# Performance work log

Hardware: AMD Instinct MI355X
Metric: run time of the kernel (lower is better)

Reference implementation:

```python
import jax, jax.numpy as jnp
import numpy as np

N = 200000      # total nodes
E = 800000      # directed edges
G = 4096        # graphs in batch
D_DRUG = 128
D_CELL = 954
HID = 128
OUT = 128
EPS = 1e-5      # BatchNorm eps


def _bn(x, gamma, beta):
    # training-mode BatchNorm1d (batch statistics, biased var), dropout is eval/identity
    m = jnp.mean(x, axis=0)
    v = jnp.mean((x - m) ** 2, axis=0)
    return gamma * (x - m) * jax.lax.rsqrt(v + EPS) + beta


def _gcn_conv(x, edge_index, W, b):
    # PyG GCNConv: add self-loops, symmetric normalization, aggregate, then bias
    src = jnp.concatenate([edge_index[0], jnp.arange(N)])
    dst = jnp.concatenate([edge_index[1], jnp.arange(N)])
    ones = jnp.ones(src.shape[0], dtype=x.dtype)
    deg = jax.ops.segment_sum(ones, dst, num_segments=N)
    dinv = jnp.where(deg > 0, jax.lax.rsqrt(jnp.maximum(deg, 1.0)), 0.0)
    norm = dinv[src] * dinv[dst]                      # [E+N]
    h = x @ W                                         # [N, out]
    msg = h[src] * norm[:, None]                      # gather + scale
    out = jax.ops.segment_sum(msg, dst, num_segments=N)  # scatter-add
    return out + b


def setup_inputs() -> dict:
    key = jax.random.key(0)
    ks = jax.random.split(key, 12)
    x = jax.random.normal(ks[0], (N, D_DRUG), jnp.float32)
    edge_index = jax.random.randint(ks[1], (2, E), 0, N)
    ibatch = (jnp.arange(N) * G) // N  # sorted, every graph non-empty
    gexpr = jax.random.normal(ks[2], (G, D_CELL), jnp.float32)

    def w(k, shape):
        return jax.random.normal(k, shape, jnp.float32) / np.float32(np.sqrt(shape[0]))

    return {
        "x": x, "edge_index": edge_index, "ibatch": ibatch, "gexpr": gexpr,
        "W1": w(ks[3], (D_DRUG, HID)), "b1": jnp.zeros((HID,), jnp.float32),
        "g1": jnp.ones((HID,), jnp.float32), "be1": jnp.zeros((HID,), jnp.float32),
        "W2": w(ks[4], (HID, OUT)), "b2": jnp.zeros((OUT,), jnp.float32),
        "g2": jnp.ones((OUT,), jnp.float32), "be2": jnp.zeros((OUT,), jnp.float32),
        "Wc1": w(ks[5], (D_CELL, HID)), "bc1": jnp.zeros((HID,), jnp.float32),
        "gc": jnp.ones((HID,), jnp.float32), "bec": jnp.zeros((HID,), jnp.float32),
        "Wc2": w(ks[6], (HID, OUT)), "bc2": jnp.zeros((OUT,), jnp.float32),
    }


def reference(x, edge_index, ibatch, gexpr,
              W1, b1, g1, be1, W2, b2, g2, be2,
              Wc1, bc1, gc, bec, Wc2, bc2):
    # drug branch
    h = _gcn_conv(x, edge_index, W1, b1)
    h = _bn(jax.nn.relu(h), g1, be1)
    h = _gcn_conv(h, edge_index, W2, b2)
    h = _bn(jax.nn.relu(h), g2, be2)
    x_drug = jax.ops.segment_max(h, ibatch, num_segments=G)  # global_max_pool
    # cellline branch
    c = jnp.tanh(gexpr @ Wc1 + bc1)
    c = _bn(c, gc, bec)
    x_cell = jax.nn.relu(c @ Wc2 + bc2)
    return x_drug, x_cell
```

## Files before the change

kernel.cpp:

```cpp
#include <hip/hip_runtime.h>

#define NFEAT 128

typedef __attribute__((ext_vector_type(4))) float f32x4;
typedef __attribute__((ext_vector_type(8))) short bf16x8;

__device__ __forceinline__ unsigned short f2bf(float f) {
    unsigned u = __builtin_bit_cast(unsigned, f);
    u += 0x7fffu + ((u >> 16) & 1u);
    return (unsigned short)(u >> 16);
}
__device__ __forceinline__ float bf2f(unsigned short s) {
    unsigned u = ((unsigned)s) << 16;
    return __builtin_bit_cast(float, u);
}

__device__ __forceinline__ void dma16(const void* g, void* l) {
    __builtin_amdgcn_global_load_lds(
        (const __attribute__((address_space(1))) unsigned int*)g,
        (__attribute__((address_space(3))) unsigned int*)l, 16, 0, 0);
}

template <int ACT, typename OutT, typename AT>
__device__ __forceinline__ void gemm_body(
    int bx, int by, const AT* __restrict__ A, const unsigned short* __restrict__ Bt,
    OutT* __restrict__ C, int M, int ldA, int ldB,
    const float* __restrict__ bias, const float* __restrict__ dscale, char* smem)
{
    constexpr bool AF32 = (sizeof(AT) == 4);
    AT* ash = (AT*)smem;
    const int tid = threadIdx.x;
    const int wv = tid >> 6, lane = tid & 63;
    const int l16 = lane & 15, quad = lane >> 4;
    const int kbase = by * 128;
    const long tile0 = (long)bx * 64;

    const int nc0 = (wv & 1) * 64;
    bf16x8 bfr[4][4];
#pragma unroll
    for (int nt = 0; nt < 4; ++nt) {
        const unsigned short* bp =
            Bt + (size_t)(nc0 + nt * 16 + l16) * ldB + kbase + quad * 8;
#pragma unroll
        for (int ks = 0; ks < 4; ++ks)
            bfr[nt][ks] = *(const bf16x8*)(bp + ks * 32);
    }

    {
        const int r0 = wv * 16;
        if constexpr (AF32) {
#pragma unroll
            for (int j = 0; j < 8; ++j) {
                const float* gp = (const float*)A +
                    (size_t)(tile0 + r0 + j * 2 + (lane >> 5)) * ldA + kbase +
                    (lane & 31) * 4;
                dma16(gp, (void*)&ash[(r0 + j * 2) * 128]);
            }
        } else {
#pragma unroll
            for (int j = 0; j < 4; ++j) {
                const unsigned short* gp = (const unsigned short*)A +
                    (size_t)(tile0 + r0 + j * 4 + (lane >> 4)) * ldA + kbase +
                    l16 * 8;
                dma16(gp, (void*)&ash[(r0 + j * 4) * 128]);
            }
        }
    }
    __syncthreads();

    const int rh = wv >> 1;
    bf16x8 af[2][4];
#pragma unroll
    for (int mt = 0; mt < 2; ++mt) {
        const int row = rh * 32 + mt * 16 + l16;
#pragma unroll
        for (int ks = 0; ks < 4; ++ks) {
            if constexpr (AF32) {
                const float* lp = (const float*)&ash[0] + row * 128 + ks * 32 + quad * 8;
                f32x4 v0 = *(const f32x4*)lp;
                f32x4 v1 = *(const f32x4*)(lp + 4);
                bf16x8 t;
                t[0] = (short)f2bf(v0[0]); t[1] = (short)f2bf(v0[1]);
                t[2] = (short)f2bf(v0[2]); t[3] = (short)f2bf(v0[3]);
                t[4] = (short)f2bf(v1[0]); t[5] = (short)f2bf(v1[1]);
                t[6] = (short)f2bf(v1[2]); t[7] = (short)f2bf(v1[3]);
                af[mt][ks] = t;
            } else {
                af[mt][ks] = *(const bf16x8*)((const unsigned short*)&ash[0] +
                                              row * 128 + ks * 32 + quad * 8);
            }
        }
    }

    f32x4 acc[2][4];
#pragma unroll
    for (int a = 0; a < 2; ++a)
#pragma unroll
        for (int b = 0; b < 4; ++b) acc[a][b] = (f32x4){0.f, 0.f, 0.f, 0.f};
#pragma unroll
    for (int ks = 0; ks < 4; ++ks)
#pragma unroll
        for (int nt = 0; nt < 4; ++nt)
#pragma unroll
            for (int mt = 0; mt < 2; ++mt)
                acc[mt][nt] = __builtin_amdgcn_mfma_f32_16x16x32_bf16(
                    af[mt][ks], bfr[nt][ks], acc[mt][nt], 0, 0, 0);

    C += (size_t)by * M * NFEAT;
    float ds[2][4];
#pragma unroll
    for (int mt = 0; mt < 2; ++mt)
#pragma unroll
        for (int r = 0; r < 4; ++r) {
            long row = tile0 + rh * 32 + mt * 16 + quad * 4 + r;
            ds[mt][r] = dscale ? dscale[row] : 1.f;
        }
#pragma unroll
    for (int nt = 0; nt < 4; ++nt) {
        int col = nc0 + nt * 16 + l16;
        float bv = bias ? bias[col] : 0.f;
#pragma unroll
        for (int mt = 0; mt < 2; ++mt) {
            long rbase = tile0 + rh * 32 + mt * 16 + quad * 4;
#pragma unroll
            for (int r = 0; r < 4; ++r) {
                float v = acc[mt][nt][r] + bv;
                if (ACT == 1) v = tanhf(v);
                if (ACT == 2) v = fmaxf(v, 0.f);
                v *= ds[mt][r];
                if constexpr (sizeof(OutT) == 2)
                    C[(size_t)(rbase + r) * NFEAT + col] = (OutT)f2bf(v);
                else
                    C[(size_t)(rbase + r) * NFEAT + col] = (OutT)v;
            }
        }
    }
}

__global__ void k_prep(const float* __restrict__ W1, unsigned short* __restrict__ W1t,
                       const float* __restrict__ Wc1, unsigned short* __restrict__ Wc1t,
                       const float* __restrict__ gexpr, float* __restrict__ Apad,
                       const int* __restrict__ dst, int* __restrict__ deg,
                       int G, int DC, int DCP, int E, int r1, int r2, int r3)
{
    int b = blockIdx.x, t = threadIdx.x;
    if (b < r1) {
        int idx = b * 256 + t;
        int n = idx >> 7, k = idx & 127;
        W1t[idx] = f2bf(W1[(size_t)k * NFEAT + n]);
    } else if (b < r2) {
        int idx = (b - r1) * 256 + t;
        int n = idx >> 10, k = idx & 1023;
        Wc1t[idx] = (k < DC) ? f2bf(Wc1[(size_t)k * NFEAT + n]) : (unsigned short)0;
    } else if (b < r3) {
        long idx = (long)(b - r2) * 256 + t;
        if (idx < (long)G * DCP) {
            long i = idx / DCP; int k = (int)(idx - i * DCP);
            Apad[idx] = (k < DC) ? gexpr[i * DC + k] : 0.f;
        }
    } else {
        int e = (b - r3) * 256 + t;
        if (e < E) atomicAdd(&deg[dst[e]], 1);
    }
}

__device__ __forceinline__ void bnfold_body(
    int bb, const float* __restrict__ sums8, const float* __restrict__ gamma,
    const float* __restrict__ beta, float invN,
    const float* __restrict__ W, const float* __restrict__ extra,
    unsigned short* __restrict__ Wt, float* __restrict__ brow)
{
    __shared__ float ssc[128], ssh[128];
    int t = threadIdx.x;
    if (t < 128) {
        float s = 0.f, s2 = 0.f;
#pragma unroll
        for (int c = 0; c < 8; ++c) { s += sums8[c * 256 + t]; s2 += sums8[c * 256 + 128 + t]; }
        float mean = s * invN;
        float var = s2 * invN - mean * mean;
        float rstd = rsqrtf(fmaxf(var, 0.f) + 1e-5f);
        float sc = gamma[t] * rstd;
        ssc[t] = sc;
        ssh[t] = beta[t] - mean * sc;
    }
    __syncthreads();
    if (bb < 64) {
        int idx = bb * 256 + t;
        int n = idx >> 7, k = idx & 127;
        Wt[idx] = f2bf(W[(size_t)k * NFEAT + n] * ssc[k]);
    } else if (t < 128) {
        float s = extra ? extra[t] : 0.f;
        for (int k = 0; k < 128; ++k) s += ssh[k] * W[(size_t)k * NFEAT + t];
        brow[t] = s;
    }
}

__global__ void k_bnfold2(
    const float* sA, const float* gA, const float* bA, float invA,
    const float* WA, const float* eA, unsigned short* WtA, float* browA,
    const float* sB, const float* gB, const float* bB, float invB,
    const float* WB, const float* eB, unsigned short* WtB, float* browB)
{
    int b = blockIdx.x;
    if (b < 65) bnfold_body(b, sA, gA, bA, invA, WA, eA, WtA, browA);
    else        bnfold_body(b - 65, sB, gB, bB, invB, WB, eB, WtB, browB);
}

__global__ __launch_bounds__(256) void k_scan1(const int* __restrict__ deg,
        int* __restrict__ rowptr, int* __restrict__ bsum, float* __restrict__ dinv, int N)
{
    __shared__ int sh[256];
    int t = threadIdx.x;
    int base = blockIdx.x * 1024 + t * 4;
    int v[4];
#pragma unroll
    for (int j = 0; j < 4; ++j) {
        v[j] = (base + j < N) ? deg[base + j] : 0;
        if (base + j < N) dinv[base + j] = rsqrtf((float)(v[j] + 1));
    }
    int s = v[0] + v[1] + v[2] + v[3];
    sh[t] = s;
    __syncthreads();
    int incl = s;
    for (int off = 1; off < 256; off <<= 1) {
        int x = (t >= off) ? sh[t - off] : 0;
        __syncthreads();
        incl += x;
        sh[t] = incl;
        __syncthreads();
    }
    int run = incl - s;
#pragma unroll
    for (int j = 0; j < 4; ++j) {
        if (base + j < N) rowptr[base + j] = run;
        run += v[j];
    }
    if (t == 255) bsum[blockIdx.x] = incl;
}

__global__ void k_scan2(int* __restrict__ bsum, int nb)
{
    __shared__ int sh[256];
    int t = threadIdx.x;
    int s = (t < nb) ? bsum[t] : 0;
    sh[t] = s;
    __syncthreads();
    int incl = s;
    for (int off = 1; off < 256; off <<= 1) {
        int x = (t >= off) ? sh[t - off] : 0;
        __syncthreads();
        incl += x;
        sh[t] = incl;
        __syncthreads();
    }
    if (t < nb) bsum[t] = incl - s;
}

__global__ void k_scan3(int* __restrict__ rowptr, int* __restrict__ cursor,
                        const int* __restrict__ bsum, int N, int E)
{
    int i = blockIdx.x * 256 + threadIdx.x;
    if (i < N) {
        int v = rowptr[i] + bsum[i >> 10];
        rowptr[i] = v;
        cursor[i] = v;
    } else if (i == N) {
        rowptr[N] = E;
    }
}

__global__ __launch_bounds__(256) void k_pair1(
    const int* __restrict__ src, const int* __restrict__ dst,
    int* __restrict__ cursor, int* __restrict__ csr, int E,
    const float* __restrict__ x, const unsigned short* __restrict__ W1t,
    unsigned short* __restrict__ h, int N, const float* __restrict__ dinv,
    const float* __restrict__ Apad, const unsigned short* __restrict__ Wc1t,
    float* __restrict__ pbuf, int G, int nf, int nd)
{
    extern __shared__ char smem[];
    int b = blockIdx.x;
    if (b < nf) {
        int e = b * 256 + threadIdx.x;
        if (e < E) {
            int pos = atomicAdd(&cursor[dst[e]], 1);
            csr[pos] = src[e];
        }
    } else if (b < nf + nd) {
        gemm_body<0, unsigned short, float>(b - nf, 0, x, W1t, h, N, 128, 128,
                                            nullptr, dinv, smem);
    } else {
        int idx = b - nf - nd;
        gemm_body<0, float, float>(idx & 63, idx >> 6, Apad, Wc1t, pbuf, G,
                                   1024, 1024, nullptr, nullptr, smem);
    }
}

__device__ __forceinline__ void unpack_add(float* acc, uint4 a)
{
    acc[0] += bf2f((unsigned short)(a.x & 0xffff));
    acc[1] += bf2f((unsigned short)(a.x >> 16));
    acc[2] += bf2f((unsigned short)(a.y & 0xffff));
    acc[3] += bf2f((unsigned short)(a.y >> 16));
    acc[4] += bf2f((unsigned short)(a.z & 0xffff));
    acc[5] += bf2f((unsigned short)(a.z >> 16));
    acc[6] += bf2f((unsigned short)(a.w & 0xffff));
    acc[7] += bf2f((unsigned short)(a.w >> 16));
}

__device__ __forceinline__ void row_gather(const unsigned short* __restrict__ h,
    const int* __restrict__ rowptr, const int* __restrict__ csr,
    long i, int f, float* acc)
{
    int lo = rowptr[i], hi = rowptr[i + 1];
    int e = lo;
    for (; e + 3 < hi; e += 4) {
        int s0 = csr[e], s1 = csr[e + 1], s2 = csr[e + 2], s3 = csr[e + 3];
        uint4 a = *(const uint4*)(h + ((size_t)s0 << 7) + f);
        uint4 b = *(const uint4*)(h + ((size_t)s1 << 7) + f);
        uint4 c = *(const uint4*)(h + ((size_t)s2 << 7) + f);
        uint4 d = *(const uint4*)(h + ((size_t)s3 << 7) + f);
        unpack_add(acc, a); unpack_add(acc, b);
        unpack_add(acc, c); unpack_add(acc, d);
    }
    for (; e < hi; ++e) {
        int s0 = csr[e];
        uint4 a = *(const uint4*)(h + ((size_t)s0 << 7) + f);
        unpack_add(acc, a);
    }
    uint4 hs = *(const uint4*)(h + ((size_t)i << 7) + f);
    unpack_add(acc, hs);
}

__global__ __launch_bounds__(256) void k_pair2(
    const unsigned short* __restrict__ h, const int* __restrict__ rowptr,
    const int* __restrict__ csr, const float* __restrict__ dinv,
    const float* __restrict__ bias, unsigned short* __restrict__ out,
    float* __restrict__ sums8, int N, int na,
    const float* __restrict__ p, const float* __restrict__ biasC,
    unsigned short* __restrict__ cbuf, float* __restrict__ sumsC, int G)
{
    __shared__ float red[4][256];
    const int tid = threadIdx.x;
    if (blockIdx.x >= na) {
        int bb = blockIdx.x - na;
        int j = tid & 127;
        int slot = bb * 2 + (tid >> 7);
        const int nslots = 64;
        const size_t st = (size_t)G * NFEAT;
        float b = biasC[j], s = 0.f, s2 = 0.f;
        for (int i = slot; i < G; i += nslots) {
            size_t o = (size_t)i * NFEAT + j;
            float v = b;
#pragma unroll
            for (int c = 0; c < 8; ++c) v += p[o + c * st];
            v = tanhf(v);
            cbuf[o] = f2bf(v);
            s += v; s2 += v * v;
        }
        atomicAdd(&sumsC[(bb & 7) * 256 + j], s);
        atomicAdd(&sumsC[(bb & 7) * 256 + 128 + j], s2);
        return;
    }
    const int wv = tid >> 6, lane = tid & 63;
    const int f = (tid & 15) << 3;
    const long g0 = (long)blockIdx.x * 16 + (tid >> 4);
    const long gstride = (long)na * 16;

    f32x4 b0 = *(const f32x4*)&bias[f];
    f32x4 b1 = *(const f32x4*)&bias[f + 4];

    float s8[8], q8[8];
#pragma unroll
    for (int j = 0; j < 8; ++j) { s8[j] = 0.f; q8[j] = 0.f; }

    for (long i = g0; i < N; i += gstride) {
        float acc[8];
#pragma unroll
        for (int j = 0; j < 8; ++j) acc[j] = 0.f;
        row_gather(h, rowptr, csr, i, f, acc);

        float di = dinv[i];
        unsigned short o[8];
#pragma unroll
        for (int j = 0; j < 8; ++j) {
            float bj = (j < 4) ? b0[j] : b1[j - 4];
            float v = fmaxf(di * acc[j] + bj, 0.f);
            o[j] = f2bf(v);
            s8[j] += v; q8[j] += v * v;
        }
        *(uint4*)(out + (i << 7) + f) = *(const uint4*)o;
    }

#pragma unroll
    for (int j = 0; j < 8; ++j) {
        s8[j] += __shfl_xor(s8[j], 16);
        s8[j] += __shfl_xor(s8[j], 32);
        q8[j] += __shfl_xor(q8[j], 16);
        q8[j] += __shfl_xor(q8[j], 32);
    }
    if (lane < 16) {
#pragma unroll
        for (int j = 0; j < 8; ++j) {
            red[wv][f + j] = s8[j];
            red[wv][128 + f + j] = q8[j];
        }
    }
    __syncthreads();
    float tot = red[0][tid] + red[1][tid] + red[2][tid] + red[3][tid];
    atomicAdd(&sums8[(blockIdx.x & 7) * 256 + tid], tot);
}

__global__ __launch_bounds__(256) void k_pair4(
    const unsigned short* __restrict__ agg, const unsigned short* __restrict__ W2t,
    unsigned short* __restrict__ h, int N, const float* __restrict__ brow2,
    const float* __restrict__ dinv,
    const unsigned short* __restrict__ cbuf, const unsigned short* __restrict__ Wc2t,
    float* __restrict__ outc, int G, const float* __restrict__ browC, int nd)
{
    extern __shared__ char smem[];
    int b = blockIdx.x;
    if (b < nd) {
        gemm_body<0, unsigned short, unsigned short>(b, 0, agg, W2t, h, N, 128, 128,
                                                     brow2, dinv, smem);
    } else {
        gemm_body<2, float, unsigned short>(b - nd, 0, cbuf, Wc2t, outc, G, 128, 128,
                                            browC, nullptr, smem);
    }
}

__global__ __launch_bounds__(256) void k_aggmax(
    const unsigned short* __restrict__ h, const int* __restrict__ rowptr,
    const int* __restrict__ csr, const float* __restrict__ dinv,
    const float* __restrict__ bias, int* __restrict__ gmax, int* __restrict__ gmin,
    float* __restrict__ sums8, int N, int G)
{
    __shared__ float red[4][256];
    __shared__ int lmax[288], lmin[288];
    const int tid = threadIdx.x;
    const int wv = tid >> 6, lane = tid & 63;
    const int f8 = tid & 15;
    const int f = f8 << 3;
    const int grp = tid >> 4;
    const int g_lo = blockIdx.x * 2;
    const int rstart = (int)(((long long)g_lo * N + G - 1) / G);
    const int rend   = (int)(((long long)(g_lo + 2) * N + G - 1) / G);
    const int bnd1   = (int)(((long long)(g_lo + 1) * N + G - 1) / G);

    for (int idx = tid; idx < 288; idx += 256) {
        lmax[idx] = 0;
        lmin[idx] = 0x7f800000;
    }
    __syncthreads();

    f32x4 b0 = *(const f32x4*)&bias[f];
    f32x4 b1 = *(const f32x4*)&bias[f + 4];

    float s8[8], q8[8], rmx[8], rmn[8];
#pragma unroll
    for (int j = 0; j < 8; ++j) {
        s8[j] = 0.f; q8[j] = 0.f;
        rmx[j] = 0.f; rmn[j] = __builtin_bit_cast(float, 0x7f800000);
    }
    int cur = 0;

    for (long i = rstart + grp; i < rend; i += 16) {
        float acc[8];
#pragma unroll
        for (int j = 0; j < 8; ++j) acc[j] = 0.f;
        row_gather(h, rowptr, csr, i, f, acc);

        float di = dinv[i];
        int gi = (i >= bnd1);
        if (gi != cur) {
#pragma unroll
            for (int j = 0; j < 8; ++j) {
                atomicMax(&lmax[cur * 144 + j * 16 + f8], __builtin_bit_cast(int, rmx[j]));
                atomicMin(&lmin[cur * 144 + j * 16 + f8], __builtin_bit_cast(int, rmn[j]));
                rmx[j] = 0.f; rmn[j] = __builtin_bit_cast(float, 0x7f800000);
            }
            cur = gi;
        }
#pragma unroll
        for (int j = 0; j < 8; ++j) {
            float bj = (j < 4) ? b0[j] : b1[j - 4];
            float v = fmaxf(di * acc[j] + bj, 0.f);
            s8[j] += v; q8[j] += v * v;
            rmx[j] = fmaxf(rmx[j], v);
            rmn[j] = fminf(rmn[j], v);
        }
    }
#pragma unroll
    for (int j = 0; j < 8; ++j) {
        atomicMax(&lmax[cur * 144 + j * 16 + f8], __builtin_bit_cast(int, rmx[j]));
        atomicMin(&lmin[cur * 144 + j * 16 + f8], __builtin_bit_cast(int, rmn[j]));
    }

#pragma unroll
    for (int j = 0; j < 8; ++j) {
        s8[j] += __shfl_xor(s8[j], 16);
        s8[j] += __shfl_xor(s8[j], 32);
        q8[j] += __shfl_xor(q8[j], 16);
        q8[j] += __shfl_xor(q8[j], 32);
    }
    if (lane < 16) {
#pragma unroll
        for (int j = 0; j < 8; ++j) {
            red[wv][f + j] = s8[j];
            red[wv][128 + f + j] = q8[j];
        }
    }
    __syncthreads();
    float tot = red[0][tid] + red[1][tid] + red[2][tid] + red[3][tid];
    atomicAdd(&sums8[(blockIdx.x & 7) * 256 + tid], tot);

    for (int idx = tid; idx < 2 * 128; idx += 256) {
        int gg = idx >> 7, feat = idx & 127;
        int a = gg * 144 + (feat & 7) * 16 + (feat >> 3);
        gmax[(size_t)(g_lo + gg) * 128 + feat] = lmax[a];
        gmin[(size_t)(g_lo + gg) * 128 + feat] = lmin[a];
    }
}

__global__ void k_segfin(const float* __restrict__ sums8, const float* __restrict__ gamma,
                         const float* __restrict__ beta, const int* __restrict__ gmax,
                         const int* __restrict__ gmin, float* __restrict__ out,
                         float invN, int total)
{
    __shared__ float ssc[128], ssh[128];
    int t = threadIdx.x;
    if (t < 128) {
        float s = 0.f, s2 = 0.f;
#pragma unroll
        for (int c = 0; c < 8; ++c) { s += sums8[c * 256 + t]; s2 += sums8[c * 256 + 128 + t]; }
        float mean = s * invN;
        float var = s2 * invN - mean * mean;
        float rstd = rsqrtf(fmaxf(var, 0.f) + 1e-5f);
        float sc = gamma[t] * rstd;
        ssc[t] = sc;
        ssh[t] = beta[t] - mean * sc;
    }
    __syncthreads();
    int idx = blockIdx.x * 256 + t;
    if (idx < total) {
        int j = idx & 127;
        float sc = ssc[j], sh = ssh[j];
        int bits = (sc >= 0.f) ? gmax[idx] : gmin[idx];
        out[idx] = sc * __builtin_bit_cast(float, bits) + sh;
    }
}

extern "C" void kernel_launch(void* const* d_in, const int* in_sizes, int n_in,
                              void* d_out, int out_size, void* d_ws, size_t ws_size,
                              hipStream_t stream)
{
    const float* x     = (const float*)d_in[0];
    const int*   ei    = (const int*)d_in[1];
    const float* gexpr = (const float*)d_in[3];
    const float* W1  = (const float*)d_in[4];
    const float* b1  = (const float*)d_in[5];
    const float* g1  = (const float*)d_in[6];
    const float* be1 = (const float*)d_in[7];
    const float* W2  = (const float*)d_in[8];
    const float* b2  = (const float*)d_in[9];
    const float* g2  = (const float*)d_in[10];
    const float* be2 = (const float*)d_in[11];
    const float* Wc1 = (const float*)d_in[12];
    const float* bc1 = (const float*)d_in[13];
    const float* gc  = (const float*)d_in[14];
    const float* bec = (const float*)d_in[15];
    const float* Wc2 = (const float*)d_in[16];
    const float* bc2 = (const float*)d_in[17];

    const int N = in_sizes[0] / NFEAT;
    const int E = in_sizes[1] / 2;
    const int G = in_sizes[3] / 954;
    const int DC = 954, DCP = 1024;

    char* wsp = (char*)d_ws;
    size_t off = 0;
    auto alloc = [&](size_t bytes) -> char* {
        char* p = wsp + off;
        off += (bytes + 255) & ~(size_t)255;
        return p;
    };
    unsigned short* agg    = (unsigned short*)alloc((size_t)N * NFEAT * 2);
    unsigned short* h      = (unsigned short*)alloc((size_t)N * NFEAT * 2);
    float*          dinv   = (float*)alloc((size_t)N * 4);
    int*            deg    = (int*)alloc((size_t)N * 4);
    int*            rowptr = (int*)alloc((size_t)(N + 1) * 4);
    int*            cursor = (int*)alloc((size_t)N * 4);
    int*            csr    = (int*)alloc((size_t)E * 4);
    int*            bsum   = (int*)alloc(256 * 4);
    float*          Apad   = (float*)alloc((size_t)G * DCP * 4);
    float*          pbuf   = (float*)alloc((size_t)8 * G * NFEAT * 4);
    unsigned short* cbuf   = (unsigned short*)alloc((size_t)G * NFEAT * 2);
    int*            gmax   = (int*)alloc((size_t)G * NFEAT * 4);
    int*            gmin   = (int*)alloc((size_t)G * NFEAT * 4);
    unsigned short* W1t    = (unsigned short*)alloc(128 * 128 * 2);
    unsigned short* W2t    = (unsigned short*)alloc(128 * 128 * 2);
    unsigned short* Wc1t   = (unsigned short*)alloc(128 * DCP * 2);
    unsigned short* Wc2t   = (unsigned short*)alloc(128 * 128 * 2);
    float*          stats  = (float*)alloc(8192 * 4);
    float* sums1 = stats,         * sums2 = stats + 2048, * sumsC = stats + 4096;
    float* brow2  = stats + 6400, * browC  = stats + 6528;

    hipMemsetAsync(stats, 0, 6144 * 4, stream);
    hipMemsetAsync(deg, 0, (size_t)N * 4, stream);

    const int* esrc = ei;
    const int* edst = ei + E;

    const int r1 = 64;
    const int r2 = r1 + 512;
    const int r3 = r2 + (int)(((long)G * DCP + 255) / 256);
    const int rtot = r3 + (E + 255) / 256;
    k_prep<<<rtot, 256, 0, stream>>>(W1, W1t, Wc1, Wc1t, gexpr, Apad,
                                     edst, deg, G, DC, DCP, E, r1, r2, r3);

    const int nb = (N + 1023) / 1024;
    k_scan1<<<nb, 256, 0, stream>>>(deg, rowptr, bsum, dinv, N);
    k_scan2<<<1, 256, 0, stream>>>(bsum, nb);
    k_scan3<<<(N + 1 + 255) / 256, 256, 0, stream>>>(rowptr, cursor, bsum, N, E);

    const int gtiles = N / 64;
    const int nf = (E + 255) / 256;
    const int ablocks = 2048;

    k_pair1<<<nf + gtiles + 512, 256, 64 * 128 * 4, stream>>>(
        esrc, edst, cursor, csr, E,
        x, W1t, h, N, dinv,
        Apad, Wc1t, pbuf, G, nf, gtiles);

    k_pair2<<<ablocks + 32, 256, 0, stream>>>(
        h, rowptr, csr, dinv, b1, agg, sums1, N, ablocks,
        pbuf, bc1, cbuf, sumsC, G);

    k_bnfold2<<<130, 256, 0, stream>>>(
        sums1, g1, be1, 1.f / (float)N, W2, nullptr, W2t, brow2,
        sumsC, gc, bec, 1.f / (float)G, Wc2, bc2, Wc2t, browC);

    float* outp = (float*)d_out;
    k_pair4<<<gtiles + G / 64, 256, 64 * 128 * 2, stream>>>(
        agg, W2t, h, N, brow2, dinv,
        cbuf, Wc2t, outp + (size_t)G * NFEAT, G, browC, gtiles);

    k_aggmax<<<G / 2, 256, 0, stream>>>(h, rowptr, csr, dinv, b2, gmax, gmin, sums2, N, G);

    k_segfin<<<(G * NFEAT + 255) / 256, 256, 0, stream>>>(
        sums2, g2, be2, gmax, gmin, outp, 1.f / (float)N, G * NFEAT);
}
```

Before: 463.4 us.

## Make GEMM blocks persistent with double-buffered LDS tile prefetch

Replaces the one-tile-per-block GEMM with a grid-stride loop in which each block loads the B fragments once and walks several 64-row tiles. The next A tile is staged into a second LDS buffer via global_load_lds while the current tile is computed. The aim is to cut per-block B reload and launch overhead and to hide load latency. In exchange LDS use doubles, which can lower occupancy, and far fewer blocks run in parallel with the edge-fill blocks. The cell-line GEMM also drops from 512 blocks to 128.

```diff
diff --git a/kernel.cpp b/kernel.cpp
--- a/kernel.cpp
+++ b/kernel.cpp
@@ -22,18 +22,19 @@
 }
 
 template <int ACT, typename OutT, typename AT>
-__device__ __forceinline__ void gemm_body(
-    int bx, int by, const AT* __restrict__ A, const unsigned short* __restrict__ Bt,
+__device__ __forceinline__ void gemm_loop(
+    int tfirst, int tstride, int tcount, int by,
+    const AT* __restrict__ A, const unsigned short* __restrict__ Bt,
     OutT* __restrict__ C, int M, int ldA, int ldB,
     const float* __restrict__ bias, const float* __restrict__ dscale, char* smem)
 {
     constexpr bool AF32 = (sizeof(AT) == 4);
-    AT* ash = (AT*)smem;
+    AT* buf0 = (AT*)smem;
+    AT* buf1 = buf0 + 64 * 128;
     const int tid = threadIdx.x;
     const int wv = tid >> 6, lane = tid & 63;
     const int l16 = lane & 15, quad = lane >> 4;
     const int kbase = by * 128;
-    const long tile0 = (long)bx * 64;
 
     const int nc0 = (wv & 1) * 64;
     bf16x8 bfr[4][4];
@@ -46,94 +47,109 @@
             bfr[nt][ks] = *(const bf16x8*)(bp + ks * 32);
     }
 
-    {
-        const int r0 = wv * 16;
+    C += (size_t)by * M * NFEAT;
+    const int rh = wv >> 1;
+    const int r0 = wv * 16;
+
+    auto stage = [&](AT* dst, long tile) {
+        const long t0 = tile * 64;
         if constexpr (AF32) {
 #pragma unroll
             for (int j = 0; j < 8; ++j) {
                 const float* gp = (const float*)A +
-                    (size_t)(tile0 + r0 + j * 2 + (lane >> 5)) * ldA + kbase +
+                    (size_t)(t0 + r0 + j * 2 + (lane >> 5)) * ldA + kbase +
                     (lane & 31) * 4;
-                dma16(gp, (void*)&ash[(r0 + j * 2) * 128]);
+                dma16(gp, (void*)&dst[(r0 + j * 2) * 128]);
             }
         } else {
 #pragma unroll
             for (int j = 0; j < 4; ++j) {
                 const unsigned short* gp = (const unsigned short*)A +
-                    (size_t)(tile0 + r0 + j * 4 + (lane >> 4)) * ldA + kbase +
+                    (size_t)(t0 + r0 + j * 4 + (lane >> 4)) * ldA + kbase +
                     l16 * 8;
-                dma16(gp, (void*)&ash[(r0 + j * 4) * 128]);
+                dma16(gp, (void*)&dst[(r0 + j * 4) * 128]);
             }
         }
-    }
-    __syncthreads();
-
-    const int rh = wv >> 1;
-    bf16x8 af[2][4];
-#pragma unroll
-    for (int mt = 0; mt < 2; ++mt) {
-        const int row = rh * 32 + mt * 16 + l16;
-#pragma unroll
-        for (int ks = 0; ks < 4; ++ks) {
-            if constexpr (AF32) {
-                const float* lp = (const float*)&ash[0] + row * 128 + ks * 32 + quad * 8;
-                f32x4 v0 = *(const f32x4*)lp;
-                f32x4 v1 = *(const f32x4*)(lp + 4);
-                bf16x8 t;
-                t[0] = (short)f2bf(v0[0]); t[1] = (short)f2bf(v0[1]);
-                t[2] = (short)f2bf(v0[2]); t[3] = (short)f2bf(v0[3]);
-                t[4] = (short)f2bf(v1[0]); t[5] = (short)f2bf(v1[1]);
-                t[6] = (short)f2bf(v1[2]); t[7] = (short)f2bf(v1[3]);
-                af[mt][ks] = t;
-            } else {
-                af[mt][ks] = *(const bf16x8*)((const unsigned short*)&ash[0] +
-                                              row * 128 + ks * 32 + quad * 8);
+    };
+
+    if (tfirst < tcount) stage(buf0, tfirst);
+    __syncthreads();
+
+    int cur = 0;
+    for (long t = tfirst; t < tcount; t += tstride) {
+        AT* bufc = cur ? buf1 : buf0;
+        AT* bufn = cur ? buf0 : buf1;
+        const long tn = t + tstride;
+        if (tn < tcount) stage(bufn, tn);
+
+        bf16x8 af[2][4];
+#pragma unroll
+        for (int mt = 0; mt < 2; ++mt) {
+            const int row = rh * 32 + mt * 16 + l16;
+#pragma unroll
+            for (int ks = 0; ks < 4; ++ks) {
+                if constexpr (AF32) {
+                    const float* lp = (const float*)bufc + row * 128 + ks * 32 + quad * 8;
+                    f32x4 v0 = *(const f32x4*)lp;
+                    f32x4 v1 = *(const f32x4*)(lp + 4);
+                    bf16x8 tt;
+                    tt[0] = (short)f2bf(v0[0]); tt[1] = (short)f2bf(v0[1]);
+                    tt[2] = (short)f2bf(v0[2]); tt[3] = (short)f2bf(v0[3]);
+                    tt[4] = (short)f2bf(v1[0]); tt[5] = (short)f2bf(v1[1]);
+                    tt[6] = (short)f2bf(v1[2]); tt[7] = (short)f2bf(v1[3]);
+                    af[mt][ks] = tt;
+                } else {
+                    af[mt][ks] = *(const bf16x8*)((const unsigned short*)bufc +
+                                                  row * 128 + ks * 32 + quad * 8);
+                }
             }
         }
-    }
-
-    f32x4 acc[2][4];
-#pragma unroll
-    for (int a = 0; a < 2; ++a)
-#pragma unroll
-        for (int b = 0; b < 4; ++b) acc[a][b] = (f32x4){0.f, 0.f, 0.f, 0.f};
-#pragma unroll
-    for (int ks = 0; ks < 4; ++ks)
-#pragma unroll
-        for (int nt = 0; nt < 4; ++nt)
-#pragma unroll
-            for (int mt = 0; mt < 2; ++mt)
-                acc[mt][nt] = __builtin_amdgcn_mfma_f32_16x16x32_bf16(
-                    af[mt][ks], bfr[nt][ks], acc[mt][nt], 0, 0, 0);
-
-    C += (size_t)by * M * NFEAT;
-    float ds[2][4];
-#pragma unroll
-    for (int mt = 0; mt < 2; ++mt)
-#pragma unroll
-        for (int r = 0; r < 4; ++r) {
-            long row = tile0 + rh * 32 + mt * 16 + quad * 4 + r;
-            ds[mt][r] = dscale ? dscale[row] : 1.f;
-        }
-#pragma unroll
-    for (int nt = 0; nt < 4; ++nt) {
-        int col = nc0 + nt * 16 + l16;
-        float bv = bias ? bias[col] : 0.f;
-#pragma unroll
-        for (int mt = 0; mt < 2; ++mt) {
-            long rbase = tile0 + rh * 32 + mt * 16 + quad * 4;
+
+        f32x4 acc[2][4];
+#pragma unroll
+        for (int a = 0; a < 2; ++a)
+#pragma unroll
+            for (int b = 0; b < 4; ++b) acc[a][b] = (f32x4){0.f, 0.f, 0.f, 0.f};
+#pragma unroll
+        for (int ks = 0; ks < 4; ++ks)
+#pragma unroll
+            for (int nt = 0; nt < 4; ++nt)
+#pragma unroll
+                for (int mt = 0; mt < 2; ++mt)
+                    acc[mt][nt] = __builtin_amdgcn_mfma_f32_16x16x32_bf16(
+                        af[mt][ks], bfr[nt][ks], acc[mt][nt], 0, 0, 0);
+
+        const long tile0 = t * 64;
+        float ds[2][4];
+#pragma unroll
+        for (int mt = 0; mt < 2; ++mt)
 #pragma unroll
             for (int r = 0; r < 4; ++r) {
-                float v = acc[mt][nt][r] + bv;
-                if (ACT == 1) v = tanhf(v);
-                if (ACT == 2) v = fmaxf(v, 0.f);
-                v *= ds[mt][r];
-                if constexpr (sizeof(OutT) == 2)
-                    C[(size_t)(rbase + r) * NFEAT + col] = (OutT)f2bf(v);
-                else
-                    C[(size_t)(rbase + r) * NFEAT + col] = (OutT)v;
+                long row = tile0 + rh * 32 + mt * 16 + quad * 4 + r;
+                ds[mt][r] = dscale ? dscale[row] : 1.f;
             }
-        }
+#pragma unroll
+        for (int nt = 0; nt < 4; ++nt) {
+            int col = nc0 + nt * 16 + l16;
+            float bv = bias ? bias[col] : 0.f;
+#pragma unroll
+            for (int mt = 0; mt < 2; ++mt) {
+                long rbase = tile0 + rh * 32 + mt * 16 + quad * 4;
+#pragma unroll
+                for (int r = 0; r < 4; ++r) {
+                    float v = acc[mt][nt][r] + bv;
+                    if (ACT == 1) v = tanhf(v);
+                    if (ACT == 2) v = fmaxf(v, 0.f);
+                    v *= ds[mt][r];
+                    if constexpr (sizeof(OutT) == 2)
+                        C[(size_t)(rbase + r) * NFEAT + col] = (OutT)f2bf(v);
+                    else
+                        C[(size_t)(rbase + r) * NFEAT + col] = (OutT)v;
+                }
+            }
+        }
+        __syncthreads();
+        cur ^= 1;
     }
 }
 
@@ -275,7 +291,7 @@
     const float* __restrict__ x, const unsigned short* __restrict__ W1t,
     unsigned short* __restrict__ h, int N, const float* __restrict__ dinv,
     const float* __restrict__ Apad, const unsigned short* __restrict__ Wc1t,
-    float* __restrict__ pbuf, int G, int nf, int nd)
+    float* __restrict__ pbuf, int G, int nf, int nb1, int gtiles)
 {
     extern __shared__ char smem[];
     int b = blockIdx.x;
@@ -285,13 +301,15 @@
             int pos = atomicAdd(&cursor[dst[e]], 1);
             csr[pos] = src[e];
         }
-    } else if (b < nf + nd) {
-        gemm_body<0, unsigned short, float>(b - nf, 0, x, W1t, h, N, 128, 128,
+    } else if (b < nf + nb1) {
+        gemm_loop<0, unsigned short, float>(b - nf, nb1, gtiles, 0,
+                                            x, W1t, h, N, 128, 128,
                                             nullptr, dinv, smem);
     } else {
-        int idx = b - nf - nd;
-        gemm_body<0, float, float>(idx & 63, idx >> 6, Apad, Wc1t, pbuf, G,
-                                   1024, 1024, nullptr, nullptr, smem);
+        int cb = b - nf - nb1;
+        gemm_loop<0, float, float>(cb & 15, 16, 64, cb >> 4,
+                                   Apad, Wc1t, pbuf, G, 1024, 1024,
+                                   nullptr, nullptr, smem);
     }
 }
 
@@ -415,15 +433,18 @@
     unsigned short* __restrict__ h, int N, const float* __restrict__ brow2,
     const float* __restrict__ dinv,
     const unsigned short* __restrict__ cbuf, const unsigned short* __restrict__ Wc2t,
-    float* __restrict__ outc, int G, const float* __restrict__ browC, int nd)
+    float* __restrict__ outc, int G, const float* __restrict__ browC,
+    int nb2, int gtiles)
 {
     extern __shared__ char smem[];
     int b = blockIdx.x;
-    if (b < nd) {
-        gemm_body<0, unsigned short, unsigned short>(b, 0, agg, W2t, h, N, 128, 128,
+    if (b < nb2) {
+        gemm_loop<0, unsigned short, unsigned short>(b, nb2, gtiles, 0,
+                                                     agg, W2t, h, N, 128, 128,
                                                      brow2, dinv, smem);
     } else {
-        gemm_body<2, float, unsigned short>(b - nd, 0, cbuf, Wc2t, outc, G, 128, 128,
+        gemm_loop<2, float, unsigned short>(b - nb2, 64, 64, 0,
+                                            cbuf, Wc2t, outc, G, 128, 128,
                                             browC, nullptr, smem);
     }
 }
@@ -625,11 +646,13 @@
     const int gtiles = N / 64;
     const int nf = (E + 255) / 256;
     const int ablocks = 2048;
-
-    k_pair1<<<nf + gtiles + 512, 256, 64 * 128 * 4, stream>>>(
+    const int NB1 = 512;
+    const int NB2 = 768;
+
+    k_pair1<<<nf + NB1 + 128, 256, 2 * 64 * 128 * 4, stream>>>(
         esrc, edst, cursor, csr, E,
         x, W1t, h, N, dinv,
-        Apad, Wc1t, pbuf, G, nf, gtiles);
+        Apad, Wc1t, pbuf, G, nf, NB1, gtiles);
 
     k_pair2<<<ablocks + 32, 256, 0, stream>>>(
         h, rowptr, csr, dinv, b1, agg, sums1, N, ablocks,
@@ -640,9 +663,9 @@
         sumsC, gc, bec, 1.f / (float)G, Wc2, bc2, Wc2t, browC);
 
     float* outp = (float*)d_out;
-    k_pair4<<<gtiles + G / 64, 256, 64 * 128 * 2, stream>>>(
+    k_pair4<<<NB2 + 64, 256, 2 * 64 * 128 * 2, stream>>>(
         agg, W2t, h, N, brow2, dinv,
-        cbuf, Wc2t, outp + (size_t)G * NFEAT, G, browC, gtiles);
+        cbuf, Wc2t, outp + (size_t)G * NFEAT, G, browC, NB2, gtiles);
 
     k_aggmax<<<G / 2, 256, 0, stream>>>(h, rowptr, csr, dinv, b2, gmax, gmin, sums2, N, G);
 
```

New measurement: 447.6 us. 1.04x faster.

## Fuse cell GEMM K-split with tanh/stats epilogue; drop LDS staging; interleave roles

Applied to the files above, without the earlier changes.

The cell-line first GEMM no longer splits K across 8 blocks into a partial-sum buffer reduced later. Each block now loops over all K chunks and applies bias, tanh, bf16 store and BN-statistic atomics in its epilogue, which removes the pbuf round trip and the reducer blocks in the aggregation kernel. The GEMM tiles now load A directly from global memory into registers instead of staging through LDS with global_load_lds, so they need no shared memory or barrier. CSR-fill and GEMM blocks are interleaved in the grid so the atomic-heavy and compute-heavy work overlap. The fused cell GEMM runs only 64 long blocks, which may serialize at the tail.

```diff
diff --git a/kernel.cpp b/kernel.cpp
--- a/kernel.cpp
+++ b/kernel.cpp
@@ -15,79 +15,51 @@
     return __builtin_bit_cast(float, u);
 }
 
-__device__ __forceinline__ void dma16(const void* g, void* l) {
-    __builtin_amdgcn_global_load_lds(
-        (const __attribute__((address_space(1))) unsigned int*)g,
-        (__attribute__((address_space(3))) unsigned int*)l, 16, 0, 0);
+__device__ __forceinline__ bf16x8 pack_bf8(f32x4 v0, f32x4 v1) {
+    bf16x8 t;
+    t[0] = (short)f2bf(v0[0]); t[1] = (short)f2bf(v0[1]);
+    t[2] = (short)f2bf(v0[2]); t[3] = (short)f2bf(v0[3]);
+    t[4] = (short)f2bf(v1[0]); t[5] = (short)f2bf(v1[1]);
+    t[6] = (short)f2bf(v1[2]); t[7] = (short)f2bf(v1[3]);
+    return t;
 }
 
 template <int ACT, typename OutT, typename AT>
-__device__ __forceinline__ void gemm_body(
-    int bx, int by, const AT* __restrict__ A, const unsigned short* __restrict__ Bt,
-    OutT* __restrict__ C, int M, int ldA, int ldB,
-    const float* __restrict__ bias, const float* __restrict__ dscale, char* smem)
+__device__ __forceinline__ void gemm_tile(
+    long tile0, const AT* __restrict__ A, const unsigned short* __restrict__ Bt,
+    OutT* __restrict__ C,
+    const float* __restrict__ bias, const float* __restrict__ dscale)
 {
     constexpr bool AF32 = (sizeof(AT) == 4);
-    AT* ash = (AT*)smem;
     const int tid = threadIdx.x;
     const int wv = tid >> 6, lane = tid & 63;
     const int l16 = lane & 15, quad = lane >> 4;
-    const int kbase = by * 128;
-    const long tile0 = (long)bx * 64;
-
     const int nc0 = (wv & 1) * 64;
+    const int rh = wv >> 1;
+
     bf16x8 bfr[4][4];
 #pragma unroll
     for (int nt = 0; nt < 4; ++nt) {
         const unsigned short* bp =
-            Bt + (size_t)(nc0 + nt * 16 + l16) * ldB + kbase + quad * 8;
+            Bt + (size_t)(nc0 + nt * 16 + l16) * NFEAT + quad * 8;
 #pragma unroll
         for (int ks = 0; ks < 4; ++ks)
             bfr[nt][ks] = *(const bf16x8*)(bp + ks * 32);
     }
 
-    {
-        const int r0 = wv * 16;
-        if constexpr (AF32) {
-#pragma unroll
-            for (int j = 0; j < 8; ++j) {
-                const float* gp = (const float*)A +
-                    (size_t)(tile0 + r0 + j * 2 + (lane >> 5)) * ldA + kbase +
-                    (lane & 31) * 4;
-                dma16(gp, (void*)&ash[(r0 + j * 2) * 128]);
-            }
-        } else {
-#pragma unroll
-            for (int j = 0; j < 4; ++j) {
-                const unsigned short* gp = (const unsigned short*)A +
-                    (size_t)(tile0 + r0 + j * 4 + (lane >> 4)) * ldA + kbase +
-                    l16 * 8;
-                dma16(gp, (void*)&ash[(r0 + j * 4) * 128]);
-            }
-        }
-    }
-    __syncthreads();
-
-    const int rh = wv >> 1;
     bf16x8 af[2][4];
 #pragma unroll
     for (int mt = 0; mt < 2; ++mt) {
-        const int row = rh * 32 + mt * 16 + l16;
+        const long row = tile0 + rh * 32 + mt * 16 + l16;
+        const AT* ap = A + (size_t)row * NFEAT + quad * 8;
 #pragma unroll
         for (int ks = 0; ks < 4; ++ks) {
             if constexpr (AF32) {
-                const float* lp = (const float*)&ash[0] + row * 128 + ks * 32 + quad * 8;
-                f32x4 v0 = *(const f32x4*)lp;
-                f32x4 v1 = *(const f32x4*)(lp + 4);
-                bf16x8 t;
-                t[0] = (short)f2bf(v0[0]); t[1] = (short)f2bf(v0[1]);
-                t[2] = (short)f2bf(v0[2]); t[3] = (short)f2bf(v0[3]);
-                t[4] = (short)f2bf(v1[0]); t[5] = (short)f2bf(v1[1]);
-                t[6] = (short)f2bf(v1[2]); t[7] = (short)f2bf(v1[3]);
-                af[mt][ks] = t;
+                f32x4 v0 = *(const f32x4*)((const float*)ap + ks * 32);
+                f32x4 v1 = *(const f32x4*)((const float*)ap + ks * 32 + 4);
+                af[mt][ks] = pack_bf8(v0, v1);
             } else {
-                af[mt][ks] = *(const bf16x8*)((const unsigned short*)&ash[0] +
-                                              row * 128 + ks * 32 + quad * 8);
+                af[mt][ks] = *(const bf16x8*)((const unsigned short*)ap + ks * 32);
             }
         }
     }
@@ -106,7 +78,6 @@
                 acc[mt][nt] = __builtin_amdgcn_mfma_f32_16x16x32_bf16(
                     af[mt][ks], bfr[nt][ks], acc[mt][nt], 0, 0, 0);
 
-    C += (size_t)by * M * NFEAT;
     float ds[2][4];
 #pragma unroll
     for (int mt = 0; mt < 2; ++mt)
@@ -133,6 +104,90 @@
                 else
                     C[(size_t)(rbase + r) * NFEAT + col] = (OutT)v;
             }
+        }
+    }
+}
+
+__device__ __forceinline__ void cell1_tile(
+    int bx, int slot, const float* __restrict__ Apad,
+    const unsigned short* __restrict__ Wc1t, unsigned short* __restrict__ cbuf,
+    const float* __restrict__ bc1, float* __restrict__ sumsC)
+{
+    const long tile0 = (long)bx * 64;
+    const int tid = threadIdx.x;
+    const int wv = tid >> 6, lane = tid & 63;
+    const int l16 = lane & 15, quad = lane >> 4;
+    const int nc0 = (wv & 1) * 64;
+    const int rh = wv >> 1;
+
+    f32x4 acc[2][4];
+#pragma unroll
+    for (int a = 0; a < 2; ++a)
+#pragma unroll
+        for (int b = 0; b < 4; ++b) acc[a][b] = (f32x4){0.f, 0.f, 0.f, 0.f};
+
+    for (int w = 0; w < 8; ++w) {
+        const int kb = w * 128;
+        bf16x8 bfr[4][4];
+#pragma unroll
+        for (int nt = 0; nt < 4; ++nt) {
+            const unsigned short* bp =
+                Wc1t + (size_t)(nc0 + nt * 16 + l16) * 1024 + kb + quad * 8;
+#pragma unroll
+            for (int ks = 0; ks < 4; ++ks)
+                bfr[nt][ks] = *(const bf16x8*)(bp + ks * 32);
+        }
+        bf16x8 af[2][4];
+#pragma unroll
+        for (int mt = 0; mt < 2; ++mt) {
+            const long row = tile0 + rh * 32 + mt * 16 + l16;
+            const float* ap = Apad + (size_t)row * 1024 + kb + quad * 8;
+#pragma unroll
+            for (int ks = 0; ks < 4; ++ks) {
+                f32x4 v0 = *(const f32x4*)(ap + ks * 32);
+                f32x4 v1 = *(const f32x4*)(ap + ks * 32 + 4);
+                af[mt][ks] = pack_bf8(v0, v1);
+            }
+        }
+#pragma unroll
+        for (int ks = 0; ks < 4; ++ks)
+#pragma unroll
+            for (int nt = 0; nt < 4; ++nt)
+#pragma unroll
+                for (int mt = 0; mt < 2; ++mt)
+                    acc[mt][nt] = __builtin_amdgcn_mfma_f32_16x16x32_bf16(
+                        af[mt][ks], bfr[nt][ks], acc[mt][nt], 0, 0, 0);
+    }
+
+    float s[4], q[4];
+#pragma unroll
+    for (int nt = 0; nt < 4; ++nt) { s[nt] = 0.f; q[nt] = 0.f; }
+#pragma unroll
+    for (int nt = 0; nt < 4; ++nt) {
+        int col = nc0 + nt * 16 + l16;
+        float bv = bc1[col];
+#pragma unroll
+        for (int mt = 0; mt < 2; ++mt) {
+            long rbase = tile0 + rh * 32 + mt * 16 + quad * 4;
+#pragma unroll
+            for (int r = 0; r < 4; ++r) {
+                float v = tanhf(acc[mt][nt][r] + bv);
+                cbuf[(size_t)(rbase + r) * NFEAT + col] = f2bf(v);
+                s[nt] += v; q[nt] += v * v;
+            }
+        }
+    }
+#pragma unroll
+    for (int nt = 0; nt < 4; ++nt) {
+        s[nt] += __shfl_xor(s[nt], 16); s[nt] += __shfl_xor(s[nt], 32);
+        q[nt] += __shfl_xor(q[nt], 16); q[nt] += __shfl_xor(q[nt], 32);
+    }
+    if (quad == 0) {
+#pragma unroll
+        for (int nt = 0; nt < 4; ++nt) {
+            int col = nc0 + nt * 16 + l16;
+            atomicAdd(&sumsC[slot * 256 + col], s[nt]);
+            atomicAdd(&sumsC[slot * 256 + 128 + col], q[nt]);
         }
     }
 }
@@ -269,29 +324,36 @@
     }
 }
 
-__global__ __launch_bounds__(256) void k_pair1(
+__global__ __launch_bounds__(256) void k_big1(
     const int* __restrict__ src, const int* __restrict__ dst,
-    int* __restrict__ cursor, int* __restrict__ csr, int E,
+    int* __restrict__ cursor, int* __restrict__ csr, int E, int nf,
     const float* __restrict__ x, const unsigned short* __restrict__ W1t,
-    unsigned short* __restrict__ h, int N, const float* __restrict__ dinv,
+    unsigned short* __restrict__ h, const float* __restrict__ dinv, int gt,
     const float* __restrict__ Apad, const unsigned short* __restrict__ Wc1t,
-    float* __restrict__ pbuf, int G, int nf, int nd)
-{
-    extern __shared__ char smem[];
-    int b = blockIdx.x;
-    if (b < nf) {
-        int e = b * 256 + threadIdx.x;
+    unsigned short* __restrict__ cbuf, const float* __restrict__ bc1,
+    float* __restrict__ sumsC)
+{
+    const int b = blockIdx.x;
+    const int nmin = (nf < gt) ? nf : gt;
+    int role, idx;
+    if (b < 2 * nmin) { role = b & 1; idx = b >> 1; }
+    else if (b < nf + gt) {
+        int r = b - 2 * nmin;
+        role = (nf > gt) ? 0 : 1;
+        idx = nmin + r;
+    } else { role = 2; idx = b - nf - gt; }
+
+    if (role == 0) {
+        int e = idx * 256 + threadIdx.x;
         if (e < E) {
             int pos = atomicAdd(&cursor[dst[e]], 1);
             csr[pos] = src[e];
         }
-    } else if (b < nf + nd) {
-        gemm_body<0, unsigned short, float>(b - nf, 0, x, W1t, h, N, 128, 128,
-                                            nullptr, dinv, smem);
+    } else if (role == 1) {
+        gemm_tile<0, unsigned short, float>((long)idx * 64, x, W1t, h,
+                                            nullptr, dinv);
     } else {
-        int idx = b - nf - nd;
-        gemm_body<0, float, float>(idx & 63, idx >> 6, Apad, Wc1t, pbuf, G,
-                                   1024, 1024, nullptr, nullptr, smem);
+        cell1_tile(idx, b & 7, Apad, Wc1t, cbuf, bc1, sumsC);
     }
 }
 
@@ -331,40 +393,18 @@
     unpack_add(acc, hs);
 }
 
-__global__ __launch_bounds__(256) void k_pair2(
+__global__ __launch_bounds__(256) void k_agg(
     const unsigned short* __restrict__ h, const int* __restrict__ rowptr,
     const int* __restrict__ csr, const float* __restrict__ dinv,
     const float* __restrict__ bias, unsigned short* __restrict__ out,
-    float* __restrict__ sums8, int N, int na,
-    const float* __restrict__ p, const float* __restrict__ biasC,
-    unsigned short* __restrict__ cbuf, float* __restrict__ sumsC, int G)
+    float* __restrict__ sums8, int N)
 {
     __shared__ float red[4][256];
     const int tid = threadIdx.x;
-    if (blockIdx.x >= na) {
-        int bb = blockIdx.x - na;
-        int j = tid & 127;
-        int slot = bb * 2 + (tid >> 7);
-        const int nslots = 64;
-        const size_t st = (size_t)G * NFEAT;
-        float b = biasC[j], s = 0.f, s2 = 0.f;
-        for (int i = slot; i < G; i += nslots) {
-            size_t o = (size_t)i * NFEAT + j;
-            float v = b;
-#pragma unroll
-            for (int c = 0; c < 8; ++c) v += p[o + c * st];
-            v = tanhf(v);
-            cbuf[o] = f2bf(v);
-            s += v; s2 += v * v;
-        }
-        atomicAdd(&sumsC[(bb & 7) * 256 + j], s);
-        atomicAdd(&sumsC[(bb & 7) * 256 + 128 + j], s2);
-        return;
-    }
     const int wv = tid >> 6, lane = tid & 63;
     const int f = (tid & 15) << 3;
     const long g0 = (long)blockIdx.x * 16 + (tid >> 4);
-    const long gstride = (long)na * 16;
+    const long gstride = (long)gridDim.x * 16;
 
     f32x4 b0 = *(const f32x4*)&bias[f];
     f32x4 b1 = *(const f32x4*)&bias[f + 4];
@@ -410,21 +450,20 @@
     atomicAdd(&sums8[(blockIdx.x & 7) * 256 + tid], tot);
 }
 
-__global__ __launch_bounds__(256) void k_pair4(
+__global__ __launch_bounds__(256) void k_big4(
     const unsigned short* __restrict__ agg, const unsigned short* __restrict__ W2t,
-    unsigned short* __restrict__ h, int N, const float* __restrict__ brow2,
-    const float* __restrict__ dinv,
+    unsigned short* __restrict__ h, const float* __restrict__ brow2,
+    const float* __restrict__ dinv, int gt,
     const unsigned short* __restrict__ cbuf, const unsigned short* __restrict__ Wc2t,
-    float* __restrict__ outc, int G, const float* __restrict__ browC, int nd)
-{
-    extern __shared__ char smem[];
-    int b = blockIdx.x;
-    if (b < nd) {
-        gemm_body<0, unsigned short, unsigned short>(b, 0, agg, W2t, h, N, 128, 128,
-                                                     brow2, dinv, smem);
+    float* __restrict__ outc, const float* __restrict__ browC)
+{
+    const int b = blockIdx.x;
+    if (b < gt) {
+        gemm_tile<0, unsigned short, unsigned short>((long)b * 64, agg, W2t, h,
+                                                     brow2, dinv);
     } else {
-        gemm_body<2, float, unsigned short>(b - nd, 0, cbuf, Wc2t, outc, G, 128, 128,
-                                            browC, nullptr, smem);
+        gemm_tile<2, float, unsigned short>((long)(b - gt) * 64, cbuf, Wc2t, outc,
+                                            browC, nullptr);
     }
 }
 
@@ -592,7 +631,6 @@
     int*            csr    = (int*)alloc((size_t)E * 4);
     int*            bsum   = (int*)alloc(256 * 4);
     float*          Apad   = (float*)alloc((size_t)G * DCP * 4);
-    float*          pbuf   = (float*)alloc((size_t)8 * G * NFEAT * 4);
     unsigned short* cbuf   = (unsigned short*)alloc((size_t)G * NFEAT * 2);
     int*            gmax   = (int*)alloc((size_t)G * NFEAT * 4);
     int*            gmin   = (int*)alloc((size_t)G * NFEAT * 4);
@@ -626,23 +664,21 @@
     const int nf = (E + 255) / 256;
     const int ablocks = 2048;
 
-    k_pair1<<<nf + gtiles + 512, 256, 64 * 128 * 4, stream>>>(
-        esrc, edst, cursor, csr, E,
-        x, W1t, h, N, dinv,
-        Apad, Wc1t, pbuf, G, nf, gtiles);
-
-    k_pair2<<<ablocks + 32, 256, 0, stream>>>(
-        h, rowptr, csr, dinv, b1, agg, sums1, N, ablocks,
-        pbuf, bc1, cbuf, sumsC, G);
+    k_big1<<<nf + gtiles + G / 64, 256, 0, stream>>>(
+        esrc, edst, cursor, csr, E, nf,
+        x, W1t, h, dinv, gtiles,
+        Apad, Wc1t, cbuf, bc1, sumsC);
+
+    k_agg<<<ablocks, 256, 0, stream>>>(h, rowptr, csr, dinv, b1, agg, sums1, N);
 
     k_bnfold2<<<130, 256, 0, stream>>>(
         sums1, g1, be1, 1.f / (float)N, W2, nullptr, W2t, brow2,
         sumsC, gc, bec, 1.f / (float)G, Wc2, bc2, Wc2t, browC);
 
     float* outp = (float*)d_out;
-    k_pair4<<<gtiles + G / 64, 256, 64 * 128 * 2, stream>>>(
-        agg, W2t, h, N, brow2, dinv,
-        cbuf, Wc2t, outp + (size_t)G * NFEAT, G, browC, gtiles);
+    k_big4<<<gtiles + G / 64, 256, 0, stream>>>(
+        agg, W2t, h, brow2, dinv, gtiles,
+        cbuf, Wc2t, outp + (size_t)G * NFEAT, browC);
 
     k_aggmax<<<G / 2, 256, 0, stream>>>(h, rowptr, csr, dinv, b2, gmax, gmin, sums2, N, G);
 
```

Result: slower. 534.8 us (+15.4%).
